# Performance work log

Measured on AMD Instinct MI355X. Metric: run time of the kernel, lower is better.

Reference implementation:

```python
import jax, jax.numpy as jnp
import numpy as np
from jax import lax

# PRPN (Parse-Read-Predict Network), eval mode (all dropout off, BatchNorm in eval
# with running stats mean=0/var=1, rmask=ones). Submodule math follows the upstream
# yikangshen/PRPN implementation vendored by jiant: ParsingNetwork (conv gate stack,
# hard hardtanh memory gates with cumprod over slots), ReadingNetwork (masked-softmax
# attention over nslots memory + LayerNorm LSTM cell, shift-append memory update),
# PredictNetwork (attention over prediction memory, res=0 -> Linear+BN+Tanh head).

T, B, V, D, H, S, L, NL = 192, 32, 50000, 384, 384, 15, 5, 2
RES = 0.1
G4 = 4 * H
BN_SC = np.float32(1.0 / np.sqrt(1.0 + 1e-5))   # eval BatchNorm with mean=0, var=1
INV_SQRT_H = np.float32(1.0 / np.sqrt(H))


def _layer_norm(x, g, b, eps=1e-6):
    # torch-style LayerNorm with unbiased std (x.std(-1))
    mu = jnp.mean(x, -1, keepdims=True)
    var = jnp.sum((x - mu) ** 2, -1, keepdims=True) / (x.shape[-1] - 1)
    return g * (x - mu) / (jnp.sqrt(var) + eps) + b


def _msoftmax(logits, gate, eps=1e-8):
    # blocks.softmax: exp-normalize then multiply by (soft) gate mask before sum
    e = jnp.exp(logits - jnp.max(logits, -1, keepdims=True)) * gate
    return e / (jnp.sum(e, -1, keepdims=True) + eps)


def _forward(input_ids, emb_w, pconv1_w, pconv1_b, pbn_g, pbn_b, pconv2_w, pconv2_b,
             r_wih, r_bih, r_whh, r_bhh, r_lnih_g, r_lnih_b, r_lnhh_g, r_lnhh_b,
             r_lnc_g, r_lnc_b, r_proj_w, r_proj_b,
             p_proj_w, p_proj_b, p_ffd_w, p_ffd_b, p_bn_g, p_bn_b):
    emb = emb_w[input_ids]                                        # (T,B,D)

    # ---- ParsingNetwork ----
    x = jnp.concatenate([jnp.zeros((L, B, D), emb.dtype), emb], 0)  # (T+L,B,D), zero history
    xc = jnp.transpose(x, (1, 2, 0))                              # (B,D,T+L)
    h1 = lax.conv_general_dilated(xc, pconv1_w, (1,), 'VALID',
                                  dimension_numbers=('NCH', 'OIH', 'NCH'))
    h1 = h1 + pconv1_b[None, :, None]
    h1 = jax.nn.relu(pbn_g[None, :, None] * h1 * BN_SC + pbn_b[None, :, None])  # (B,H,T)
    half = H // 2
    # Conv1d(nhid, 2, 1, groups=2): channel 0 from first half, channel 1 from second
    gate = jax.nn.sigmoid(jnp.einsum('bct,c->bt', h1[:, :half], pconv2_w[0]) + pconv2_b[0])
    gate_next = jax.nn.sigmoid(jnp.einsum('bct,c->bt', h1[:, half:], pconv2_w[1]) + pconv2_b[1])
    cum = jnp.concatenate([jnp.full((B, S), 1e9, gate.dtype), gate], 1)  # init cum_gate = +inf
    gate_hat = jnp.stack([cum[:, S - k:S - k + T] for k in range(S)], 2)  # (B,T,S)

    def mem_gate(g):  # hard gates: (hardtanh((g-ghat)/res*2+1)+1)/2, cumprod over slots
        u = (jnp.clip((g[:, :, None] - gate_hat) / RES * 2.0 + 1.0, -1.0, 1.0) + 1.0) * 0.5
        return jnp.cumprod(u, axis=2)

    mg = jnp.transpose(mem_gate(gate), (1, 0, 2))                 # (T,B,S)
    mgn = jnp.transpose(mem_gate(gate_next), (1, 0, 2))           # (T,B,S)

    # ---- per-timestep Read / Predict-attention loop ----
    def step(carry, xs):
        mem_h, mem_c, pmem = carry       # (NL,B,S,H),(NL,B,S,H),(B,S,H)
        e_t, mg_t, mgn_t = xs
        h = e_t
        nh, nc = [], []
        for j in range(NL):
            mh, mc = mem_h[j], mem_c[j]
            key_j = jnp.concatenate([h, mh[:, -1]], -1) @ r_proj_w[j].T + r_proj_b[j]
            att = _msoftmax(jnp.einsum('bsh,bh->bs', mh, key_j) * INV_SQRT_H, mg_t)
            sel_h = jnp.einsum('bs,bsh->bh', att, mh)
            sel_c = jnp.einsum('bs,bsh->bh', att, mc)
            gates = (_layer_norm(h @ r_wih[j].T + r_bih[j], r_lnih_g[j], r_lnih_b[j])
                     + _layer_norm(sel_h @ r_whh[j].T + r_bhh[j], r_lnhh_g[j], r_lnhh_b[j]))
            i_g, f_g, c_g, o_g = jnp.split(gates, 4, axis=-1)
            c_new = jax.nn.sigmoid(f_g) * sel_c + jax.nn.sigmoid(i_g) * jnp.tanh(c_g)
            h_new = jax.nn.sigmoid(o_g) * jnp.tanh(_layer_norm(c_new, r_lnc_g[j], r_lnc_b[j]))
            nh.append(jnp.concatenate([mh[:, 1:], h_new[:, None]], 1))
            nc.append(jnp.concatenate([mc[:, 1:], c_new[:, None]], 1))
            h = h_new
        pkey = jnp.concatenate([h, pmem[:, -1]], -1) @ p_proj_w.T + p_proj_b
        patt = _msoftmax(jnp.einsum('bsh,bh->bs', pmem, pkey) * INV_SQRT_H, mgn_t)
        sel = jnp.einsum('bs,bsh->bh', patt, pmem)
        pmem_new = jnp.concatenate([pmem[:, 1:], h[:, None]], 1)
        return (jnp.stack(nh), jnp.stack(nc), pmem_new), (h, sel)

    carry0 = (jnp.zeros((NL, B, S, H), emb.dtype),
              jnp.zeros((NL, B, S, H), emb.dtype),
              jnp.zeros((B, S, H), emb.dtype))
    _, (out_h, out_sel) = lax.scan(step, carry0, (emb, mg, mgn))

    # ---- PredictNetwork head (res=0): Linear(2H->D) + BN(eval) + Tanh ----
    flat = jnp.concatenate([out_h.reshape(T * B, H), out_sel.reshape(T * B, H)], -1)
    y = flat @ p_ffd_w.T + p_ffd_b
    y = jnp.tanh(p_bn_g * y * BN_SC + p_bn_b)
    return y.reshape(T, B, D)


def setup_inputs() -> dict:
    key = jax.random.key(0)
    ks = iter(jax.random.split(key, 16))

    def rn(shape, s=0.05):
        return jax.random.normal(next(ks), shape, dtype=jnp.float32) * s

    return {
        "input_ids": jax.random.randint(next(ks), (T, B), 0, V),
        "emb_w": rn((V, D), 0.01),
        "pconv1_w": rn((H, D, L + 1)),
        "pconv1_b": jnp.zeros((H,), jnp.float32),
        "pbn_g": jnp.ones((H,), jnp.float32),
        "pbn_b": jnp.zeros((H,), jnp.float32),
        "pconv2_w": rn((2, H // 2)),
        "pconv2_b": jnp.zeros((2,), jnp.float32),
        "r_wih": rn((NL, G4, D)),
        "r_bih": jnp.zeros((NL, G4), jnp.float32),
        "r_whh": rn((NL, G4, H)),
        "r_bhh": jnp.zeros((NL, G4), jnp.float32),
        "r_lnih_g": jnp.ones((NL, G4), jnp.float32),
        "r_lnih_b": jnp.zeros((NL, G4), jnp.float32),
        "r_lnhh_g": jnp.ones((NL, G4), jnp.float32),
        "r_lnhh_b": jnp.zeros((NL, G4), jnp.float32),
        "r_lnc_g": jnp.ones((NL, H), jnp.float32),
        "r_lnc_b": jnp.zeros((NL, H), jnp.float32),
        "r_proj_w": rn((NL, H, D + H)),
        "r_proj_b": jnp.zeros((NL, H), jnp.float32),
        "p_proj_w": rn((H, 2 * H)),
        "p_proj_b": jnp.zeros((H,), jnp.float32),
        "p_ffd_w": rn((D, 2 * H)),
        "p_ffd_b": jnp.zeros((D,), jnp.float32),
        "p_bn_g": jnp.ones((D,), jnp.float32),
        "p_bn_b": jnp.zeros((D,), jnp.float32),
    }


def reference(input_ids, emb_w, pconv1_w, pconv1_b, pbn_g, pbn_b, pconv2_w, pconv2_b,
              r_wih, r_bih, r_whh, r_bhh, r_lnih_g, r_lnih_b, r_lnhh_g, r_lnhh_b,
              r_lnc_g, r_lnc_b, r_proj_w, r_proj_b,
              p_proj_w, p_proj_b, p_ffd_w, p_ffd_b, p_bn_g, p_bn_b):
    out = _forward(input_ids, emb_w, pconv1_w, pconv1_b, pbn_g, pbn_b, pconv2_w, pconv2_b,
                   r_wih, r_bih, r_whh, r_bhh, r_lnih_g, r_lnih_b, r_lnhh_g, r_lnhh_b,
                   r_lnc_g, r_lnc_b, r_proj_w, r_proj_b,
                   p_proj_w, p_proj_b, p_ffd_w, p_ffd_b, p_bn_g, p_bn_b)
    mask = input_ids != 0
    return out, mask
```

## Files before the change

### kernel.cpp

```cpp
#include <hip/hip_runtime.h>


#define TT 192
#define TB 6144

constexpr size_t O_EMB    = 0;
constexpr size_t O_IH0LN  = 2359296;
constexpr size_t O_KEY0E  = 11796480;
constexpr size_t O_MG     = 14155776;
constexpr size_t O_MGN    = 14247936;
constexpr size_t O_H1     = 14340096;
constexpr size_t O_GATEA  = 16699392;
constexpr size_t O_GATEB  = 16705536;
constexpr size_t O_OUTHS  = 16711680;
constexpr size_t O_MEMH0  = 21430272;
constexpr size_t O_MEMC0  = 21614592;
constexpr size_t O_MEMH1  = 21798912;
constexpr size_t O_MEMC1  = 21983232;
constexpr size_t O_PMEM   = 22167552;
constexpr size_t O_P0     = 22351872;
constexpr size_t O_P1     = 23089152;
constexpr size_t O_HNEW0  = 23826432;
constexpr size_t O_HNEW1  = 23838720;
constexpr size_t O_IH1RAW = 23851008;
constexpr size_t O_KEY1H  = 23900160;
constexpr size_t O_KEY0MH = 23912448;
constexpr size_t O_KEY1MH = 23924736;
constexpr size_t O_PKEYH  = 23937024;
constexpr size_t O_PKEYMH = 23949312;
constexpr size_t O_BAR    = 23973888;
constexpr size_t O_WSEND  = 23974432;

__device__ __forceinline__ float sigmoidf(float x) { return 1.f / (1.f + expf(-x)); }

__device__ __forceinline__ float ldx(const float* p) {
  return __hip_atomic_load(p, __ATOMIC_RELAXED, __HIP_MEMORY_SCOPE_AGENT);
}
__device__ __forceinline__ void stx(float* p, float v) {
  __hip_atomic_store(p, v, __ATOMIC_RELAXED, __HIP_MEMORY_SCOPE_AGENT);
}
__device__ __forceinline__ unsigned ldu(const unsigned* p) {
  return __hip_atomic_load(p, __ATOMIC_RELAXED, __HIP_MEMORY_SCOPE_AGENT);
}

constexpr float BN_SC = 0.9999950000374997f;
constexpr float INV_SQRT_H = 0.05103103630798288f;

__device__ __forceinline__ float blockSum(float v, float* red) {
#pragma unroll
  for (int off = 32; off > 0; off >>= 1) v += __shfl_down(v, off, 64);
  __syncthreads();
  if ((threadIdx.x & 63) == 0) red[threadIdx.x >> 6] = v;
  __syncthreads();
  return red[0] + red[1] + red[2] + red[3];
}

__global__ __launch_bounds__(256) void k_zero(float* p, int n) {
  int i = blockIdx.x * 256 + threadIdx.x;
  int stride = gridDim.x * 256;
  for (; i < n; i += stride) p[i] = 0.f;
}

__global__ __launch_bounds__(256) void k_emb(const int* ids, const float* emb_w,
                                             float* emb, float* out) {
  size_t idx = (size_t)blockIdx.x * 256 + threadIdx.x;
  size_t stride = (size_t)gridDim.x * 256;
  for (size_t i = idx; i < (size_t)TB * 384; i += stride) {
    size_t tb = i / 384, d = i - tb * 384;
    int id = ids[tb];
    emb[i] = emb_w[(size_t)id * 384 + d];
    if (i < TB) out[(size_t)TB * 384 + i] = (ids[i] != 0) ? 1.f : 0.f;
  }
}

__global__ __launch_bounds__(256) void k_conv(const float* emb, const float* W1, const float* cbias,
                                              const float* bng, const float* bnb, float* h1) {
  __shared__ float As[32][68];
  __shared__ float Bs[32][68];
  int n0 = blockIdx.x * 64, m0 = blockIdx.y * 64;
  int tid = threadIdx.x;
  float acc[4][4] = {};
  int mi = tid >> 3, kq = tid & 7;
  int ni = tid >> 2, kb = tid & 3;
  for (int kk = 0; kk < 2304; kk += 32) {
    int kc = kk / 384, dbase = kk - kc * 384;
    __syncthreads();
#pragma unroll
    for (int p = 0; p < 2; ++p) {
      int m = m0 + mi + 32 * p;
      int b = m / 192, t = m - b * 192;
      int tt = t + kc - 5;
      float4 v = {0.f, 0.f, 0.f, 0.f};
      if (tt >= 0) v = *(const float4*)(emb + ((size_t)tt * 32 + b) * 384 + dbase + kq * 4);
      As[kq * 4 + 0][mi + 32 * p] = v.x; As[kq * 4 + 1][mi + 32 * p] = v.y;
      As[kq * 4 + 2][mi + 32 * p] = v.z; As[kq * 4 + 3][mi + 32 * p] = v.w;
    }
#pragma unroll
    for (int i = 0; i < 8; ++i) {
      int d = dbase + kb * 8 + i;
      Bs[kb * 8 + i][ni] = W1[(size_t)(n0 + ni) * 2304 + d * 6 + kc];
    }
    __syncthreads();
    int ty = tid >> 4, tx = tid & 15;
#pragma unroll
    for (int k = 0; k < 32; ++k) {
      float4 a = *(const float4*)(&As[k][ty * 4]);
      float4 bv = *(const float4*)(&Bs[k][tx * 4]);
// ... 93 lines not shown
  }
  int ty = tid >> 4, tx = tid & 15;
#pragma unroll
  for (int i = 0; i < 4; ++i) {
    int m = m0 + ty * 4 + i;
#pragma unroll
    for (int j = 0; j < 4; ++j) {
      int n = n0 + tx * 4 + j;
      float v = acc[i][j];
      if (bias) v += bias[n];
      if (mode == 0) Cf[(size_t)m * ldc + n] = v;
      else Cb[(size_t)m * ldc + n] = tanhf(bng[n] * v * BN_SC + bnb[n]);
    }
  }
}

__global__ __launch_bounds__(256) void k_ln_rows(float* X, const float* g, const float* bt) {
  __shared__ float red[8];
  float* x = X + (size_t)blockIdx.x * 1536;
  int tid = threadIdx.x;
  float ps = 0.f;
  for (int i = tid; i < 1536; i += 256) ps += x[i];
  float mu = blockSum(ps, red) * (1.f / 1536.f);
  ps = 0.f;
  for (int i = tid; i < 1536; i += 256) { float d = x[i] - mu; ps += d * d; }
  float inv = 1.f / (sqrtf(blockSum(ps, red) * (1.f / 1535.f)) + 1e-6f);
  for (int i = tid; i < 1536; i += 256) x[i] = g[i] * (x[i] - mu) * inv + bt[i];
}

struct ScanArgs {
  float* ws;
  const float *r_whh, *r_bhh, *r_lnhh_g, *r_lnhh_b, *r_lnih_g, *r_lnih_b;
  const float *r_lnc_g, *r_lnc_b, *r_wih, *r_bih, *r_proj_w, *r_proj_b;
  const float *p_proj_w, *p_proj_b;
};

struct GJob { const float* W; int ldw; int koff; const float* bias; float* dst; int rstride; int ncols; };

__device__ __forceinline__ void resolveJob(const GJob* J, int col, const float*& W, int& ldw, int& koff,
                                           const float*& bias, float*& dst, int& rstride, int& cc) {
  int c = col;
#pragma unroll
  for (int j = 0; j < 4; ++j) {
    if (c < J[j].ncols) {
      W = J[j].W; ldw = J[j].ldw; koff = J[j].koff; bias = J[j].bias;
      dst = J[j].dst; rstride = J[j].rstride; cc = c; return;
    }
    c -= J[j].ncols;
  }
  W = J[0].W; ldw = J[0].ldw; koff = J[0].koff; bias = J[0].bias;
  dst = J[0].dst; rstride = J[0].rstride; cc = 0;
}

__device__ void grid_barrier(unsigned* bar, int wg, unsigned k) {
  __syncthreads();
  if (threadIdx.x == 0) {
    const int g = wg >> 4;
    unsigned arr = __hip_atomic_fetch_add(bar + g * 16, 1u, __ATOMIC_RELAXED, __HIP_MEMORY_SCOPE_AGENT);
    if (arr == k * 16u + 15u) {
      unsigned ra = __hip_atomic_fetch_add(bar + 256, 1u, __ATOMIC_RELAXED, __HIP_MEMORY_SCOPE_AGENT);
      if (ra == k * 16u + 15u) {
        __hip_atomic_store(bar + 272, k + 1u, __ATOMIC_RELAXED, __HIP_MEMORY_SCOPE_AGENT);
      } else {
        while (ldu(bar + 272) < k + 1u) __builtin_amdgcn_s_sleep(2);
      }
      __hip_atomic_store(bar + 288 + g * 16, k + 1u, __ATOMIC_RELAXED, __HIP_MEMORY_SCOPE_AGENT);
    } else {
      while (ldu(bar + 288 + g * 16) < k + 1u) __builtin_amdgcn_s_sleep(8);
    }
  }
  __syncthreads();
}

#define NG_GEMV 224
__device__ void gemm_phase(const float* src, const GJob* J, int NC, int gwg,
                           float* xs , float* red ) {
  const int tid = threadIdx.x;
  for (int j = tid; j < 12288; j += 256) {
    int bb = j >> 8;
    bb = j / 384;
    int kk = j - bb * 384;
    xs[bb * 385 + kk] = ldx(src + j);
  }
  __syncthreads();
  const int b = tid & 31, cg = tid >> 5;
  const int c0 = (gwg * NC) / NG_GEMV, c1 = ((gwg + 1) * NC) / NG_GEMV;
  const int colsPer = c1 - c0;
  const int k0 = cg * 48;
  float xr[48];
  const float* xp = xs + b * 385 + k0;
#pragma unroll
  for (int q = 0; q < 48; ++q) xr[q] = xp[q];
  for (int ci = 0; ci < colsPer; ++ci) {
    const float* W; int ldw, koff; const float* bias; float* dst; int rstride; int cc;
    resolveJob(J, c0 + ci, W, ldw, koff, bias, dst, rstride, cc);
    const float* wr = W + (size_t)cc * ldw + koff + k0;
    float a = 0.f;
#pragma unroll
    for (int q = 0; q < 12; ++q) {
      float4 w = *(const float4*)(wr + q * 4);
      a += w.x * xr[q * 4 + 0] + w.y * xr[q * 4 + 1]
         + w.z * xr[q * 4 + 2] + w.w * xr[q * 4 + 3];
    }
    red[(cg * colsPer + ci) * 33 + b] = a;
  }
  __syncthreads();
  const int pairs = colsPer * 32;
  for (int pi = tid; pi < pairs; pi += 256) {
    int bb = pi / colsPer, ci = pi - bb * colsPer;
    float s = 0.f;
#pragma unroll
    for (int g = 0; g < 8; ++g) s += red[(g * colsPer + ci) * 33 + bb];
    const float* W; int ldw, koff; const float* bias; float* dst; int rstride; int cc;
    resolveJob(J, c0 + ci, W, ldw, koff, bias, dst, rstride, cc);
    if (bias) s += bias[cc];
    stx(dst + (size_t)bb * rstride + cc, s);
  }
  __syncthreads();
}

__device__ void per_b_layer(int layer, int t, int b, const ScanArgs& A, float* sm) {
  float* ws = A.ws;
  const int tid = threadIdx.x;
  const size_t tb = (size_t)t * 32 + b;
  float* memh = ws + (layer ? O_MEMH1 : O_MEMH0) + (size_t)b * 15 * 384;
  float* memc = ws + (layer ? O_MEMC1 : O_MEMC0) + (size_t)b * 15 * 384;
  float* P = ws + (layer ? O_P1 : O_P0) + (size_t)b * 15 * 1536;
  float* keyl = sm; float* logit = sm + 384; float* att = sm + 400; float* red = sm + 416;
  float* ghh = sm + 448; float* gih = sm + 1984; float* selc = sm + 3520;
  float* cnew = sm + 3904; float* ogat = sm + 4288;

  for (int h = tid; h < 384; h += 256) {
    float k1, k2;
    if (layer == 0) { k1 = ws[O_KEY0E + tb * 384 + h]; k2 = ldx(ws + O_KEY0MH + (size_t)b * 384 + h); }
    else { k1 = ldx(ws + O_KEY1H + (size_t)b * 384 + h); k2 = ldx(ws + O_KEY1MH + (size_t)b * 384 + h); }
    keyl[h] = k1 + k2;
  }
  __syncthreads();
  {
    int s = tid >> 4, l = tid & 15;
    if (s < 15) {
      const float* mh = memh + ((t + s) % 15) * 384;
      float p = 0.f;
      for (int k = l; k < 384; k += 16) p += mh[k] * keyl[k];
      p += __shfl_down(p, 8, 64); p += __shfl_down(p, 4, 64);
      p += __shfl_down(p, 2, 64); p += __shfl_down(p, 1, 64);
      if (l == 0) logit[s] = p * INV_SQRT_H;
    }
  }
  __syncthreads();
  if (tid == 0) {
    const float* mgp = ws + O_MG + tb * 15;
    float m = logit[0];
    for (int i = 1; i < 15; ++i) m = fmaxf(m, logit[i]);
    float sum = 0.f;
    for (int i = 0; i < 15; ++i) { float e = expf(logit[i] - m) * mgp[i]; att[i] = e; sum += e; }
    float inv = 1.f / (sum + 1e-8f);
    for (int i = 0; i < 15; ++i) att[i] *= inv;
  }
  __syncthreads();
  float av[15]; int pidx[15];
#pragma unroll
  for (int i = 0; i < 15; ++i) { av[i] = att[i]; pidx[i] = (t + i) % 15; }
  const float* bhh = A.r_bhh + layer * 1536;
  for (int n = tid; n < 1536; n += 256) {
    float acc = bhh[n];
#pragma unroll
    for (int i = 0; i < 15; ++i) acc += av[i] * ldx(P + (size_t)pidx[i] * 1536 + n);
    ghh[n] = acc;
  }
  for (int h = tid; h < 384; h += 256) {
    float acc = 0.f;
#pragma unroll
    for (int i = 0; i < 15; ++i) acc += av[i] * memc[pidx[i] * 384 + h];
    selc[h] = acc;
  }
  if (layer) {
    for (int n = tid; n < 1536; n += 256) gih[n] = ldx(ws + O_IH1RAW + (size_t)b * 1536 + n);
  }
  __syncthreads();
  float ps = 0.f;
  for (int n = tid; n < 1536; n += 256) ps += ghh[n];
  float mu_hh = blockSum(ps, red) * (1.f / 1536.f);
  ps = 0.f;
  for (int n = tid; n < 1536; n += 256) { float d = ghh[n] - mu_hh; ps += d * d; }
  float inv_hh = 1.f / (sqrtf(blockSum(ps, red) * (1.f / 1535.f)) + 1e-6f);
  float mu_ih = 0.f, inv_ih = 0.f;
  if (layer) {
    ps = 0.f;
    for (int n = tid; n < 1536; n += 256) ps += gih[n];
    mu_ih = blockSum(ps, red) * (1.f / 1536.f);
    ps = 0.f;
    for (int n = tid; n < 1536; n += 256) { float d = gih[n] - mu_ih; ps += d * d; }
    inv_ih = 1.f / (sqrtf(blockSum(ps, red) * (1.f / 1535.f)) + 1e-6f);
  }
  const float *hg = A.r_lnhh_g + layer * 1536, *hb = A.r_lnhh_b + layer * 1536;
  const float *ig = A.r_lnih_g + 1536, *ib = A.r_lnih_b + 1536;
  for (int h = tid; h < 384; h += 256) {
    float gi, gf, gc, go;
    if (layer == 0) {
      const float* ihr = ws + O_IH0LN + tb * 1536;
      gi = ihr[h]; gf = ihr[384 + h]; gc = ihr[768 + h]; go = ihr[1152 + h];
    } else {
      gi = ig[h] * (gih[h] - mu_ih) * inv_ih + ib[h];
      gf = ig[384 + h] * (gih[384 + h] - mu_ih) * inv_ih + ib[384 + h];
      gc = ig[768 + h] * (gih[768 + h] - mu_ih) * inv_ih + ib[768 + h];
      go = ig[1152 + h] * (gih[1152 + h] - mu_ih) * inv_ih + ib[1152 + h];
    }
    gi += hg[h] * (ghh[h] - mu_hh) * inv_hh + hb[h];
    gf += hg[384 + h] * (ghh[384 + h] - mu_hh) * inv_hh + hb[384 + h];
    gc += hg[768 + h] * (ghh[768 + h] - mu_hh) * inv_hh + hb[768 + h];
    go += hg[1152 + h] * (ghh[1152 + h] - mu_hh) * inv_hh + hb[1152 + h];
    float c = sigmoidf(gf) * selc[h] + sigmoidf(gi) * tanhf(gc);
    cnew[h] = c; ogat[h] = go;
  }
  __syncthreads();
  ps = 0.f;
  for (int h = tid; h < 384; h += 256) ps += cnew[h];
  float mu_c = blockSum(ps, red) * (1.f / 384.f);
  ps = 0.f;
  for (int h = tid; h < 384; h += 256) { float d = cnew[h] - mu_c; ps += d * d; }
  float inv_c = 1.f / (sqrtf(blockSum(ps, red) * (1.f / 383.f)) + 1e-6f);
  const float *lcg = A.r_lnc_g + layer * 384, *lcb = A.r_lnc_b + layer * 384;
  const int slot = t % 15;
  for (int h = tid; h < 384; h += 256) {
    float hn = sigmoidf(ogat[h]) * tanhf(lcg[h] * (cnew[h] - mu_c) * inv_c + lcb[h]);
    memh[slot * 384 + h] = hn;
    memc[slot * 384 + h] = cnew[h];
    if (layer == 0) stx(ws + O_HNEW0 + (size_t)b * 384 + h, hn);
    else { stx(ws + O_HNEW1 + (size_t)b * 384 + h, hn); ws[O_OUTHS + tb * 768 + h] = hn; }
  }
}

__device__ void per_b_predict(int tau, int b, const ScanArgs& A, float* sm) {
  float* ws = A.ws;
  const int tid = threadIdx.x;
  const size_t tb = (size_t)tau * 32 + b;
  float* pmem = ws + O_PMEM + (size_t)b * 15 * 384;
  float* keyl = sm; float* logit = sm + 384; float* att = sm + 400;
  for (int h = tid; h < 384; h += 256)
    keyl[h] = ldx(ws + O_PKEYH + (size_t)b * 384 + h)
            + ldx(ws + O_PKEYMH + (size_t)(tau & 1) * 12288 + (size_t)b * 384 + h);
  __syncthreads();
  {
    int s = tid >> 4, l = tid & 15;
    if (s < 15) {
      const float* mh = pmem + ((tau + s) % 15) * 384;
      float p = 0.f;
      for (int k = l; k < 384; k += 16) p += mh[k] * keyl[k];
      p += __shfl_down(p, 8, 64); p += __shfl_down(p, 4, 64);
      p += __shfl_down(p, 2, 64); p += __shfl_down(p, 1, 64);
      if (l == 0) logit[s] = p * INV_SQRT_H;
    }
  }
  __syncthreads();
  if (tid == 0) {
    const float* mgp = ws + O_MGN + tb * 15;
    float m = logit[0];
    for (int i = 1; i < 15; ++i) m = fmaxf(m, logit[i]);
    float sum = 0.f;
    for (int i = 0; i < 15; ++i) { float e = expf(logit[i] - m) * mgp[i]; att[i] = e; sum += e; }
    float inv = 1.f / (sum + 1e-8f);
    for (int i = 0; i < 15; ++i) att[i] *= inv;
  }
  __syncthreads();
  float av[15]; int pidx[15];
#pragma unroll
  for (int i = 0; i < 15; ++i) { av[i] = att[i]; pidx[i] = (tau + i) % 15; }
  for (int h = tid; h < 384; h += 256) {
    float acc = 0.f;
#pragma unroll
    for (int i = 0; i < 15; ++i) acc += av[i] * pmem[pidx[i] * 384 + h];
    ws[O_OUTHS + tb * 768 + 384 + h] = acc;
  }
  __syncthreads();
  for (int h = tid; h < 384; h += 256)
    pmem[(tau % 15) * 384 + h] = ldx(ws + O_HNEW1 + (size_t)b * 384 + h);
}

__global__ __launch_bounds__(256) void k_scan(ScanArgs A) {
  __shared__ float sm[16032];
  float* ws = A.ws;
  unsigned* bar = (unsigned*)(ws + O_BAR);
  const int wg = blockIdx.x;
  float* xs = sm;
  float* red = sm + 12320;
  unsigned bk = 0;
  for (int t = 0; t <= TT; ++t) {
    if (wg < 32) {
      if (t < TT) per_b_layer(0, t, wg, A, sm);
    } else {
      GJob J[4] = {
        { A.r_whh + 589824, 384, 0, nullptr, ws + O_P1 + (size_t)((t + 14) % 15) * 1536, 23040, 1536 },
        { A.r_proj_w + 294912, 768, 384, nullptr, ws + O_KEY1MH, 384, 384 },
        { A.p_proj_w, 768, 0, A.p_proj_b, ws + O_PKEYH, 384, 384 },
        { A.p_proj_w, 768, 384, nullptr, ws + O_PKEYMH + (size_t)(t & 1) * 12288, 384, 384 },
      };
      gemm_phase(ws + O_HNEW1, J, 2688, wg - 32, xs, red);
    }
    grid_barrier(bar, wg, bk); ++bk;
    if (wg < 32) {
      if (t >= 1) per_b_predict(t - 1, wg, A, sm);
    } else if (t < TT) {
      GJob J[4] = {
        { A.r_wih + 589824, 384, 0, A.r_bih + 1536, ws + O_IH1RAW, 1536, 1536 },
        { A.r_proj_w + 294912, 768, 0, A.r_proj_b + 384, ws + O_KEY1H, 384, 384 },
        { nullptr, 0, 0, nullptr, nullptr, 0, 0 },
        { nullptr, 0, 0, nullptr, nullptr, 0, 0 },
      };
      gemm_phase(ws + O_HNEW0, J, 1920, wg - 32, xs, red);
    }
    if (t == TT) break;
    grid_barrier(bar, wg, bk); ++bk;
    if (wg < 32) {
      per_b_layer(1, t, wg, A, sm);
    } else {
      GJob J[4] = {
        { A.r_whh, 384, 0, nullptr, ws + O_P0 + (size_t)(t % 15) * 1536, 23040, 1536 },
        { A.r_proj_w, 768, 384, nullptr, ws + O_KEY0MH, 384, 384 },
        { nullptr, 0, 0, nullptr, nullptr, 0, 0 },
        { nullptr, 0, 0, nullptr, nullptr, 0, 0 },
      };
      gemm_phase(ws + O_HNEW0, J, 1920, wg - 32, xs, red);
    }
    grid_barrier(bar, wg, bk); ++bk;
  }
}

extern "C" void kernel_launch(void* const* d_in, const int* in_sizes, int n_in,
                              void* d_out, int out_size, void* d_ws, size_t ws_size,
                              hipStream_t stream) {
  const int* ids = (const int*)d_in[0];
  const float* emb_w = (const float*)d_in[1];
  const float* pconv1_w = (const float*)d_in[2];
  const float* pconv1_b = (const float*)d_in[3];
  const float* pbn_g = (const float*)d_in[4];
  const float* pbn_b = (const float*)d_in[5];
  const float* pconv2_w = (const float*)d_in[6];
  const float* pconv2_b = (const float*)d_in[7];
  const float* r_wih = (const float*)d_in[8];
  const float* r_bih = (const float*)d_in[9];
  const float* r_whh = (const float*)d_in[10];
  const float* r_bhh = (const float*)d_in[11];
  const float* r_lnih_g = (const float*)d_in[12];
  const float* r_lnih_b = (const float*)d_in[13];
  const float* r_lnhh_g = (const float*)d_in[14];
  const float* r_lnhh_b = (const float*)d_in[15];
  const float* r_lnc_g = (const float*)d_in[16];
  const float* r_lnc_b = (const float*)d_in[17];
  const float* r_proj_w = (const float*)d_in[18];
  const float* r_proj_b = (const float*)d_in[19];
  const float* p_proj_w = (const float*)d_in[20];
  const float* p_proj_b = (const float*)d_in[21];
  const float* p_ffd_w = (const float*)d_in[22];
  const float* p_ffd_b = (const float*)d_in[23];
  const float* p_bn_g = (const float*)d_in[24];
  const float* p_bn_b = (const float*)d_in[25];
  float* ws = (float*)d_ws;
  float* out = (float*)d_out;

  k_zero<<<1024, 256, 0, stream>>>(ws + O_MEMH0, (int)(O_WSEND - O_MEMH0));
  k_emb<<<4096, 256, 0, stream>>>(ids, emb_w, ws + O_EMB, out);
  k_conv<<<dim3(6, 96), 256, 0, stream>>>(ws + O_EMB, pconv1_w, pconv1_b, pbn_g, pbn_b, ws + O_H1);
  k_gate<<<6144, 256, 0, stream>>>(ws + O_H1, pconv2_w, pconv2_b, ws + O_GATEA, ws + O_GATEB);
  k_mg<<<24, 256, 0, stream>>>(ws + O_GATEA, ws + O_GATEB, ws + O_MG, ws + O_MGN);
  k_gemm<<<dim3(24, 96), 256, 0, stream>>>(ws + O_EMB, 384, r_wih, 384, r_bih,
                                           ws + O_IH0LN, 1536, 384, 0, nullptr, nullptr, nullptr);
  k_gemm<<<dim3(6, 96), 256, 0, stream>>>(ws + O_EMB, 384, r_proj_w, 768, r_proj_b,
                                          ws + O_KEY0E, 384, 384, 0, nullptr, nullptr, nullptr);
  k_ln_rows<<<6144, 256, 0, stream>>>(ws + O_IH0LN, r_lnih_g, r_lnih_b);
  ScanArgs SA{ws, r_whh, r_bhh, r_lnhh_g, r_lnhh_b, r_lnih_g, r_lnih_b,
              r_lnc_g, r_lnc_b, r_wih, r_bih, r_proj_w, r_proj_b, p_proj_w, p_proj_b};
  k_scan<<<256, 256, 0, stream>>>(SA);
  k_gemm<<<dim3(6, 96), 256, 0, stream>>>(ws + O_OUTHS, 768, p_ffd_w, 768, p_ffd_b,
                                          nullptr, 384, 768, 1, p_bn_g, p_bn_b, out);
}
```

Before: 14.24 ms.

## Pipeline LSTM layers and predict across workgroup sets with split producer/consumer barriers

New measurement: 16.21 ms. +13.9%, slower.

```diff
diff --git a/kernel.cpp b/kernel.cpp
--- a/kernel.cpp
+++ b/kernel.cpp
@@ -3,6 +3,7 @@
 
 #define TT 192
 #define TB 6144
+#define NGV 160
 
 constexpr size_t O_EMB    = 0;
 constexpr size_t O_IH0LN  = 2359296;
@@ -21,7 +22,8 @@
 constexpr size_t O_P0     = 22351872;
 constexpr size_t O_P1     = 23089152;
 constexpr size_t O_HNEW0  = 23826432;
-constexpr size_t O_HNEW1  = 23838720;
+constexpr size_t O_HNEW1A = 23838720;
+constexpr size_t O_HNEW1B = 14340096;
 constexpr size_t O_IH1RAW = 23851008;
 constexpr size_t O_KEY1H  = 23900160;
 constexpr size_t O_KEY0MH = 23912448;
@@ -30,6 +32,13 @@
 constexpr size_t O_PKEYMH = 23949312;
 constexpr size_t O_BAR    = 23973888;
 constexpr size_t O_WSEND  = 23974432;
+
+#define BO_GRP_E  0
+#define BO_ROOT_E 96
+#define BO_GEN_E  112
+#define BO_GRP_O  128
+#define BO_ROOT_O 288
+#define BO_GEN_O  304
 
 __device__ __forceinline__ float sigmoidf(float x) { return 1.f / (1.f + expf(-x)); }
 
@@ -252,49 +261,28 @@
   dst = J[0].dst; rstride = J[0].rstride; cc = 0;
 }
 
-__device__ void grid_barrier(unsigned* bar, int wg, unsigned k) {
-  __syncthreads();
-  if (threadIdx.x == 0) {
-    const int g = wg >> 4;
-    unsigned arr = __hip_atomic_fetch_add(bar + g * 16, 1u, __ATOMIC_RELAXED, __HIP_MEMORY_SCOPE_AGENT);
-    if (arr == k * 16u + 15u) {
-      unsigned ra = __hip_atomic_fetch_add(bar + 256, 1u, __ATOMIC_RELAXED, __HIP_MEMORY_SCOPE_AGENT);
-      if (ra == k * 16u + 15u) {
-        __hip_atomic_store(bar + 272, k + 1u, __ATOMIC_RELAXED, __HIP_MEMORY_SCOPE_AGENT);
-      } else {
-        while (ldu(bar + 272) < k + 1u) __builtin_amdgcn_s_sleep(2);
-      }
-      __hip_atomic_store(bar + 288 + g * 16, k + 1u, __ATOMIC_RELAXED, __HIP_MEMORY_SCOPE_AGENT);
-    } else {
-      while (ldu(bar + 288 + g * 16) < k + 1u) __builtin_amdgcn_s_sleep(8);
-    }
-  }
-  __syncthreads();
-}
-
-#define NG_GEMV 224
-__device__ void gemm_phase(const float* src, const GJob* J, int NC, int gwg,
-                           float* xs , float* red ) {
+__device__ __forceinline__ void arrive2(unsigned* bar, int grpOff, int rootOff, int genOff,
+                                        int g, int ngroups, unsigned s) {
+  unsigned a = __hip_atomic_fetch_add(bar + grpOff + g * 16, 1u, __ATOMIC_RELAXED, __HIP_MEMORY_SCOPE_AGENT);
+  if (a == s * 16u + 15u) {
+    unsigned r = __hip_atomic_fetch_add(bar + rootOff, 1u, __ATOMIC_RELAXED, __HIP_MEMORY_SCOPE_AGENT);
+    if (r == s * (unsigned)ngroups + (unsigned)(ngroups - 1))
+      __hip_atomic_store(bar + genOff, s + 1u, __ATOMIC_RELAXED, __HIP_MEMORY_SCOPE_AGENT);
+  }
+}
+__device__ __forceinline__ void waitgen(const unsigned* bar, int genOff, unsigned tgt) {
+  while (ldu(bar + genOff) < tgt) __builtin_amdgcn_s_sleep(2);
+}
+
+__device__ void gemv_half(const GJob* J, int NC, int gwg, const float* xr, float* red) {
   const int tid = threadIdx.x;
-  for (int j = tid; j < 12288; j += 256) {
-    int bb = j >> 8;
-    bb = j / 384;
-    int kk = j - bb * 384;
-    xs[bb * 385 + kk] = ldx(src + j);
-  }
-  __syncthreads();
   const int b = tid & 31, cg = tid >> 5;
-  const int c0 = (gwg * NC) / NG_GEMV, c1 = ((gwg + 1) * NC) / NG_GEMV;
-  const int colsPer = c1 - c0;
-  const int k0 = cg * 48;
-  float xr[48];
-  const float* xp = xs + b * 385 + k0;
-#pragma unroll
-  for (int q = 0; q < 48; ++q) xr[q] = xp[q];
-  for (int ci = 0; ci < colsPer; ++ci) {
+  const int c0 = (gwg * NC) / NGV, c1 = ((gwg + 1) * NC) / NGV;
+  const int nch = c1 - c0;
+  for (int ci = 0; ci < nch; ++ci) {
     const float* W; int ldw, koff; const float* bias; float* dst; int rstride; int cc;
     resolveJob(J, c0 + ci, W, ldw, koff, bias, dst, rstride, cc);
-    const float* wr = W + (size_t)cc * ldw + koff + k0;
+    const float* wr = W + (size_t)cc * ldw + koff + cg * 48;
     float a = 0.f;
 #pragma unroll
     for (int q = 0; q < 12; ++q) {
@@ -302,19 +290,20 @@
       a += w.x * xr[q * 4 + 0] + w.y * xr[q * 4 + 1]
          + w.z * xr[q * 4 + 2] + w.w * xr[q * 4 + 3];
     }
-    red[(cg * colsPer + ci) * 33 + b] = a;
-  }
-  __syncthreads();
-  const int pairs = colsPer * 32;
+    a += __shfl_down(a, 32, 64);
+    if ((cg & 1) == 0) red[((cg >> 1) * nch + ci) * 33 + b] = a;
+  }
+  __syncthreads();
+  const int pairs = nch * 32;
   for (int pi = tid; pi < pairs; pi += 256) {
-    int bb = pi / colsPer, ci = pi - bb * colsPer;
-    float s = 0.f;
-#pragma unroll
-    for (int g = 0; g < 8; ++g) s += red[(g * colsPer + ci) * 33 + bb];
+    int bb = pi / nch, ci = pi - bb * nch;
+    float ssum = 0.f;
+#pragma unroll
+    for (int g2 = 0; g2 < 4; ++g2) ssum += red[(g2 * nch + ci) * 33 + bb];
     const float* W; int ldw, koff; const float* bias; float* dst; int rstride; int cc;
     resolveJob(J, c0 + ci, W, ldw, koff, bias, dst, rstride, cc);
-    if (bias) s += bias[cc];
-    stx(dst + (size_t)bb * rstride + cc, s);
+    if (bias) ssum += bias[cc];
+    stx(dst + (size_t)bb * rstride + cc, ssum);
   }
   __syncthreads();
 }
@@ -336,6 +325,11 @@
     else { k1 = ldx(ws + O_KEY1H + (size_t)b * 384 + h); k2 = ldx(ws + O_KEY1MH + (size_t)b * 384 + h); }
     keyl[h] = k1 + k2;
   }
+  if (layer) {
+    for (int n = tid; n < 1536; n += 256) gih[n] = ldx(ws + O_IH1RAW + (size_t)b * 1536 + n);
+  } else {
+    for (int n = tid; n < 1536; n += 256) gih[n] = ws[O_IH0LN + tb * 1536 + n];
+  }
   __syncthreads();
   {
     int s = tid >> 4, l = tid & 15;
@@ -374,9 +368,6 @@
 #pragma unroll
     for (int i = 0; i < 15; ++i) acc += av[i] * memc[pidx[i] * 384 + h];
     selc[h] = acc;
-  }
-  if (layer) {
-    for (int n = tid; n < 1536; n += 256) gih[n] = ldx(ws + O_IH1RAW + (size_t)b * 1536 + n);
   }
   __syncthreads();
   float ps = 0.f;
@@ -399,8 +390,7 @@
   for (int h = tid; h < 384; h += 256) {
     float gi, gf, gc, go;
     if (layer == 0) {
-      const float* ihr = ws + O_IH0LN + tb * 1536;
-      gi = ihr[h]; gf = ihr[384 + h]; gc = ihr[768 + h]; go = ihr[1152 + h];
+      gi = gih[h]; gf = gih[384 + h]; gc = gih[768 + h]; go = gih[1152 + h];
     } else {
       gi = ig[h] * (gih[h] - mu_ih) * inv_ih + ib[h];
       gf = ig[384 + h] * (gih[384 + h] - mu_ih) * inv_ih + ib[384 + h];
@@ -427,8 +417,12 @@
     float hn = sigmoidf(ogat[h]) * tanhf(lcg[h] * (cnew[h] - mu_c) * inv_c + lcb[h]);
     memh[slot * 384 + h] = hn;
     memc[slot * 384 + h] = cnew[h];
-    if (layer == 0) stx(ws + O_HNEW0 + (size_t)b * 384 + h, hn);
-    else { stx(ws + O_HNEW1 + (size_t)b * 384 + h, hn); ws[O_OUTHS + tb * 768 + h] = hn; }
+    if (layer == 0) {
+      stx(ws + O_HNEW0 + (size_t)b * 384 + h, hn);
+    } else {
+      stx(ws + ((t & 1) ? O_HNEW1B : O_HNEW1A) + (size_t)b * 384 + h, hn);
+      ws[O_OUTHS + tb * 768 + h] = hn;
+    }
   }
 }
 
@@ -475,55 +469,101 @@
   }
   __syncthreads();
   for (int h = tid; h < 384; h += 256)
-    pmem[(tau % 15) * 384 + h] = ldx(ws + O_HNEW1 + (size_t)b * 384 + h);
+    pmem[(tau % 15) * 384 + h] = ldx(ws + ((tau & 1) ? O_HNEW1B : O_HNEW1A) + (size_t)b * 384 + h);
 }
 
 __global__ __launch_bounds__(256) void k_scan(ScanArgs A) {
-  __shared__ float sm[16032];
+  __shared__ float sm[15488];
   float* ws = A.ws;
   unsigned* bar = (unsigned*)(ws + O_BAR);
   const int wg = blockIdx.x;
-  float* xs = sm;
-  float* red = sm + 12320;
-  unsigned bk = 0;
-  for (int t = 0; t <= TT; ++t) {
-    if (wg < 32) {
-      if (t < TT) per_b_layer(0, t, wg, A, sm);
-    } else {
-      GJob J[4] = {
-        { A.r_whh + 589824, 384, 0, nullptr, ws + O_P1 + (size_t)((t + 14) % 15) * 1536, 23040, 1536 },
-        { A.r_proj_w + 294912, 768, 384, nullptr, ws + O_KEY1MH, 384, 384 },
-        { A.p_proj_w, 768, 0, A.p_proj_b, ws + O_PKEYH, 384, 384 },
-        { A.p_proj_w, 768, 384, nullptr, ws + O_PKEYMH + (size_t)(t & 1) * 12288, 384, 384 },
-      };
-      gemm_phase(ws + O_HNEW1, J, 2688, wg - 32, xs, red);
-    }
-    grid_barrier(bar, wg, bk); ++bk;
-    if (wg < 32) {
-      if (t >= 1) per_b_predict(t - 1, wg, A, sm);
-    } else if (t < TT) {
-      GJob J[4] = {
-        { A.r_wih + 589824, 384, 0, A.r_bih + 1536, ws + O_IH1RAW, 1536, 1536 },
-        { A.r_proj_w + 294912, 768, 0, A.r_proj_b + 384, ws + O_KEY1H, 384, 384 },
-        { nullptr, 0, 0, nullptr, nullptr, 0, 0 },
-        { nullptr, 0, 0, nullptr, nullptr, 0, 0 },
-      };
-      gemm_phase(ws + O_HNEW0, J, 1920, wg - 32, xs, red);
-    }
-    if (t == TT) break;
-    grid_barrier(bar, wg, bk); ++bk;
-    if (wg < 32) {
-      per_b_layer(1, t, wg, A, sm);
-    } else {
-      GJob J[4] = {
-        { A.r_whh, 384, 0, nullptr, ws + O_P0 + (size_t)(t % 15) * 1536, 23040, 1536 },
-        { A.r_proj_w, 768, 384, nullptr, ws + O_KEY0MH, 384, 384 },
-        { nullptr, 0, 0, nullptr, nullptr, 0, 0 },
-        { nullptr, 0, 0, nullptr, nullptr, 0, 0 },
-      };
-      gemm_phase(ws + O_HNEW0, J, 1920, wg - 32, xs, red);
-    }
-    grid_barrier(bar, wg, bk); ++bk;
+  const int tid = threadIdx.x;
+
+  if (wg < 96) {
+    const int g = wg >> 4;
+    for (int s = 0; s < 194; ++s) {
+      if (wg < 32) {
+        if (s < 192) per_b_layer(0, s, wg, A, sm);
+      } else if (wg < 64) {
+        if (s >= 1 && s <= 192) per_b_layer(1, s - 1, wg - 32, A, sm);
+      } else {
+        if (s >= 2) per_b_predict(s - 2, wg - 64, A, sm);
+      }
+      __syncthreads();
+      if (tid == 0) {
+        arrive2(bar, BO_GRP_E, BO_ROOT_E, BO_GEN_E, g, 6, (unsigned)s);
+        if (s < 193) waitgen(bar, BO_GEN_O, (unsigned)s + 1);
+      }
+      __syncthreads();
+    }
+  } else {
+    const int gwg = wg - 96;
+    const int g = gwg >> 4;
+    float* xs = sm;
+    float* red = sm + 12320;
+    const int b = tid & 31, cg = tid >> 5;
+    const float* xp = xs + b * 385 + cg * 48;
+    for (int s = 0; s < 193; ++s) {
+      if (tid == 0) waitgen(bar, BO_GEN_E, (unsigned)s + 1);
+      __syncthreads();
+      const bool doG0 = (s < 192), doG1 = (s >= 1);
+      const float* src1 = ws + (((s - 1) & 1) ? O_HNEW1B : O_HNEW1A);
+      float xr[48];
+      if (doG0) {
+        for (int j = tid; j < 12288; j += 256) {
+          int bb = j / 384, kk = j - bb * 384;
+          xs[bb * 385 + kk] = ldx(ws + O_HNEW0 + j);
+        }
+        __syncthreads();
+#pragma unroll
+        for (int q = 0; q < 48; ++q) xr[q] = xp[q];
+        float x1v[48];
+        if (doG1) {
+#pragma unroll
+          for (int q = 0; q < 48; ++q) x1v[q] = ldx(src1 + tid + q * 256);
+        }
+        __syncthreads();
+        {
+          GJob J0[4] = {
+            { A.r_wih + 589824, 384, 0, A.r_bih + 1536, ws + O_IH1RAW, 1536, 1536 },
+            { A.r_proj_w + 294912, 768, 0, A.r_proj_b + 384, ws + O_KEY1H, 384, 384 },
+            { A.r_whh, 384, 0, nullptr, ws + O_P0 + (size_t)(s % 15) * 1536, 23040, 1536 },
+            { A.r_proj_w, 768, 384, nullptr, ws + O_KEY0MH, 384, 384 },
+          };
+          gemv_half(J0, 3840, gwg, xr, red);
+        }
+        if (doG1) {
+#pragma unroll
+          for (int q = 0; q < 48; ++q) {
+            int j = tid + q * 256;
+            int bb = j / 384, kk = j - bb * 384;
+            xs[bb * 385 + kk] = x1v[q];
+          }
+          __syncthreads();
+#pragma unroll
+          for (int q = 0; q < 48; ++q) xr[q] = xp[q];
+        }
+      } else {
+        for (int j = tid; j < 12288; j += 256) {
+          int bb = j / 384, kk = j - bb * 384;
+          xs[bb * 385 + kk] = ldx(src1 + j);
+        }
+        __syncthreads();
+#pragma unroll
+        for (int q = 0; q < 48; ++q) xr[q] = xp[q];
+      }
+      if (doG1) {
+        GJob J1[4] = {
+          { A.r_whh + 589824, 384, 0, nullptr, ws + O_P1 + (size_t)((s + 14) % 15) * 1536, 23040, 1536 },
+          { A.r_proj_w + 294912, 768, 384, nullptr, ws + O_KEY1MH, 384, 384 },
+          { A.p_proj_w, 768, 0, A.p_proj_b, ws + O_PKEYH, 384, 384 },
+          { A.p_proj_w, 768, 384, nullptr, ws + O_PKEYMH + (size_t)(s & 1) * 12288, 384, 384 },
+        };
+        gemv_half(J1, 2688, gwg, xr, red);
+      }
+      __syncthreads();
+      if (tid == 0) arrive2(bar, BO_GRP_O, BO_ROOT_O, BO_GEN_O, g, 10, (unsigned)s);
+    }
   }
 }
 
```

## Split scan workgroups by role, stage gate GEMV outputs, and vectorize per-batch steps

Applied to the files above, without the earlier changes.

Result: no change. 14.31 ms (+0.5%).

```diff
diff --git a/kernel.cpp b/kernel.cpp
--- a/kernel.cpp
+++ b/kernel.cpp
@@ -3,6 +3,7 @@
 
 #define TT 192
 #define TB 6144
+#define NGV 192
 
 constexpr size_t O_EMB    = 0;
 constexpr size_t O_IH0LN  = 2359296;
@@ -10,6 +11,8 @@
 constexpr size_t O_MG     = 14155776;
 constexpr size_t O_MGN    = 14247936;
 constexpr size_t O_H1     = 14340096;
+constexpr size_t O_P0S    = 14340096;
+constexpr size_t O_P1S    = 14389248;
 constexpr size_t O_GATEA  = 16699392;
 constexpr size_t O_GATEB  = 16705536;
 constexpr size_t O_OUTHS  = 16711680;
@@ -39,6 +42,15 @@
 __device__ __forceinline__ void stx(float* p, float v) {
   __hip_atomic_store(p, v, __ATOMIC_RELAXED, __HIP_MEMORY_SCOPE_AGENT);
 }
+__device__ __forceinline__ float2 ldx2(const float* p) {
+  unsigned long long v = __hip_atomic_load((const unsigned long long*)p,
+                                           __ATOMIC_RELAXED, __HIP_MEMORY_SCOPE_AGENT);
+  return __builtin_bit_cast(float2, v);
+}
+__device__ __forceinline__ void stx2(float* p, float2 v) {
+  __hip_atomic_store((unsigned long long*)p, __builtin_bit_cast(unsigned long long, v),
+                     __ATOMIC_RELAXED, __HIP_MEMORY_SCOPE_AGENT);
+}
 __device__ __forceinline__ unsigned ldu(const unsigned* p) {
   return __hip_atomic_load(p, __ATOMIC_RELAXED, __HIP_MEMORY_SCOPE_AGENT);
 }
@@ -53,6 +65,19 @@
   if ((threadIdx.x & 63) == 0) red[threadIdx.x >> 6] = v;
   __syncthreads();
   return red[0] + red[1] + red[2] + red[3];
+}
+
+__device__ __forceinline__ float2 blockSum2(float a, float b, float* red) {
+#pragma unroll
+  for (int off = 32; off > 0; off >>= 1) {
+    a += __shfl_down(a, off, 64);
+    b += __shfl_down(b, off, 64);
+  }
+  __syncthreads();
+  if ((threadIdx.x & 63) == 0) { int w = threadIdx.x >> 6; red[2 * w] = a; red[2 * w + 1] = b; }
+  __syncthreads();
+  return make_float2(red[0] + red[2] + red[4] + red[6],
+                     red[1] + red[3] + red[5] + red[7]);
 }
 
 __global__ __launch_bounds__(256) void k_zero(float* p, int n) {
@@ -266,25 +291,24 @@
       }
       __hip_atomic_store(bar + 288 + g * 16, k + 1u, __ATOMIC_RELAXED, __HIP_MEMORY_SCOPE_AGENT);
     } else {
-      while (ldu(bar + 288 + g * 16) < k + 1u) __builtin_amdgcn_s_sleep(8);
-    }
-  }
-  __syncthreads();
-}
-
-#define NG_GEMV 224
-__device__ void gemm_phase(const float* src, const GJob* J, int NC, int gwg,
+      while (ldu(bar + 288 + g * 16) < k + 1u) __builtin_amdgcn_s_sleep(4);
+    }
+  }
+  __syncthreads();
+}
+
+__device__ void gemv_phase(const float* src, const GJob* J, int NC, int gwg,
                            float* xs , float* red ) {
   const int tid = threadIdx.x;
-  for (int j = tid; j < 12288; j += 256) {
-    int bb = j >> 8;
-    bb = j / 384;
-    int kk = j - bb * 384;
-    xs[bb * 385 + kk] = ldx(src + j);
+  for (int j2 = tid; j2 < 6144; j2 += 256) {
+    int j = j2 * 2;
+    int bb = j / 384, kk = j - bb * 384;
+    float2 v = ldx2(src + j);
+    xs[bb * 385 + kk] = v.x; xs[bb * 385 + kk + 1] = v.y;
   }
   __syncthreads();
   const int b = tid & 31, cg = tid >> 5;
-  const int c0 = (gwg * NC) / NG_GEMV, c1 = ((gwg + 1) * NC) / NG_GEMV;
+  const int c0 = (gwg * NC) / NGV, c1 = ((gwg + 1) * NC) / NGV;
   const int colsPer = c1 - c0;
   const int k0 = cg * 48;
   float xr[48];
@@ -319,23 +343,56 @@
   __syncthreads();
 }
 
+__device__ void preload_l0(int t, int b, const ScanArgs& A, float* sm) {
+  float* ws = A.ws;
+  const int tid = threadIdx.x;
+  const size_t tb = (size_t)t * 32 + b;
+  float* keyl = sm; float* gih = sm + 1984;
+  for (int n = tid; n < 1536; n += 256) gih[n] = ws[O_IH0LN + tb * 1536 + n];
+  if (tid < 192) {
+    float2 v = *(const float2*)(ws + O_KEY0E + tb * 384 + 2 * tid);
+    keyl[2 * tid] = v.x; keyl[2 * tid + 1] = v.y;
+  }
+}
+
 __device__ void per_b_layer(int layer, int t, int b, const ScanArgs& A, float* sm) {
   float* ws = A.ws;
   const int tid = threadIdx.x;
   const size_t tb = (size_t)t * 32 + b;
   float* memh = ws + (layer ? O_MEMH1 : O_MEMH0) + (size_t)b * 15 * 384;
   float* memc = ws + (layer ? O_MEMC1 : O_MEMC0) + (size_t)b * 15 * 384;
-  float* P = ws + (layer ? O_P1 : O_P0) + (size_t)b * 15 * 1536;
+  float* mir  = ws + (layer ? O_P1 : O_P0) + (size_t)b * 23040;
+  const float* stg = ws + (layer ? O_P1S : O_P0S) + (size_t)b * 1536;
   float* keyl = sm; float* logit = sm + 384; float* att = sm + 400; float* red = sm + 416;
   float* ghh = sm + 448; float* gih = sm + 1984; float* selc = sm + 3520;
   float* cnew = sm + 3904; float* ogat = sm + 4288;
 
-  for (int h = tid; h < 384; h += 256) {
-    float k1, k2;
-    if (layer == 0) { k1 = ws[O_KEY0E + tb * 384 + h]; k2 = ldx(ws + O_KEY0MH + (size_t)b * 384 + h); }
-    else { k1 = ldx(ws + O_KEY1H + (size_t)b * 384 + h); k2 = ldx(ws + O_KEY1MH + (size_t)b * 384 + h); }
-    keyl[h] = k1 + k2;
-  }
+  const int pslot = (t + 14) % 15;
+#pragma unroll
+  for (int i = 0; i < 3; ++i) {
+    int idx = tid + i * 256;
+    float2 v = ldx2(stg + 2 * idx);
+    *(float2*)(mir + (size_t)pslot * 1536 + 2 * idx) = v;
+  }
+  if (layer == 0) {
+    if (tid < 192) {
+      float2 c = ldx2(ws + O_KEY0MH + (size_t)b * 384 + 2 * tid);
+      keyl[2 * tid] += c.x; keyl[2 * tid + 1] += c.y;
+    }
+  } else {
+#pragma unroll
+    for (int i = 0; i < 3; ++i) {
+      int idx = tid + i * 256;
+      float2 v = ldx2(ws + O_IH1RAW + (size_t)b * 1536 + 2 * idx);
+      gih[2 * idx] = v.x; gih[2 * idx + 1] = v.y;
+    }
+    if (tid < 192) {
+      float2 a = ldx2(ws + O_KEY1H + (size_t)b * 384 + 2 * tid);
+      float2 c = ldx2(ws + O_KEY1MH + (size_t)b * 384 + 2 * tid);
+      keyl[2 * tid] = a.x + c.x; keyl[2 * tid + 1] = a.y + c.y;
+    }
+  }
+  float mgv = (tid < 15) ? ws[O_MG + tb * 15 + tid] : 0.f;
   __syncthreads();
   {
     int s = tid >> 4, l = tid & 15;
@@ -349,14 +406,17 @@
     }
   }
   __syncthreads();
-  if (tid == 0) {
-    const float* mgp = ws + O_MG + tb * 15;
-    float m = logit[0];
-    for (int i = 1; i < 15; ++i) m = fmaxf(m, logit[i]);
-    float sum = 0.f;
-    for (int i = 0; i < 15; ++i) { float e = expf(logit[i] - m) * mgp[i]; att[i] = e; sum += e; }
-    float inv = 1.f / (sum + 1e-8f);
-    for (int i = 0; i < 15; ++i) att[i] *= inv;
+  if (tid < 64) {
+    float lg = (tid < 15) ? logit[tid] : -3.0e38f;
+    lg = fmaxf(lg, __shfl_xor(lg, 8, 64));
+    lg = fmaxf(lg, __shfl_xor(lg, 4, 64));
+    lg = fmaxf(lg, __shfl_xor(lg, 2, 64));
+    lg = fmaxf(lg, __shfl_xor(lg, 1, 64));
+    float e = (tid < 15) ? expf(logit[tid] - lg) * mgv : 0.f;
+    float ssum = e;
+    ssum += __shfl_xor(ssum, 1, 64); ssum += __shfl_xor(ssum, 2, 64);
+    ssum += __shfl_xor(ssum, 4, 64); ssum += __shfl_xor(ssum, 8, 64);
+    if (tid < 15) att[tid] = e / (ssum + 1e-8f);
   }
   __syncthreads();
   float av[15]; int pidx[15];
@@ -366,7 +426,7 @@
   for (int n = tid; n < 1536; n += 256) {
     float acc = bhh[n];
 #pragma unroll
-    for (int i = 0; i < 15; ++i) acc += av[i] * ldx(P + (size_t)pidx[i] * 1536 + n);
+    for (int i = 0; i < 15; ++i) acc += av[i] * mir[(size_t)pidx[i] * 1536 + n];
     ghh[n] = acc;
   }
   for (int h = tid; h < 384; h += 256) {
@@ -375,32 +435,26 @@
     for (int i = 0; i < 15; ++i) acc += av[i] * memc[pidx[i] * 384 + h];
     selc[h] = acc;
   }
-  if (layer) {
-    for (int n = tid; n < 1536; n += 256) gih[n] = ldx(ws + O_IH1RAW + (size_t)b * 1536 + n);
-  }
-  __syncthreads();
-  float ps = 0.f;
-  for (int n = tid; n < 1536; n += 256) ps += ghh[n];
-  float mu_hh = blockSum(ps, red) * (1.f / 1536.f);
-  ps = 0.f;
-  for (int n = tid; n < 1536; n += 256) { float d = ghh[n] - mu_hh; ps += d * d; }
-  float inv_hh = 1.f / (sqrtf(blockSum(ps, red) * (1.f / 1535.f)) + 1e-6f);
+  __syncthreads();
+  float s1 = 0.f, s2 = 0.f;
+  for (int n = tid; n < 1536; n += 256) { float v = ghh[n]; s1 += v; s2 += v * v; }
+  float2 rhh = blockSum2(s1, s2, red);
+  float mu_hh = rhh.x * (1.f / 1536.f);
+  float inv_hh = 1.f / (sqrtf(fmaxf(rhh.y - rhh.x * mu_hh, 0.f) * (1.f / 1535.f)) + 1e-6f);
   float mu_ih = 0.f, inv_ih = 0.f;
   if (layer) {
-    ps = 0.f;
-    for (int n = tid; n < 1536; n += 256) ps += gih[n];
-    mu_ih = blockSum(ps, red) * (1.f / 1536.f);
-    ps = 0.f;
-    for (int n = tid; n < 1536; n += 256) { float d = gih[n] - mu_ih; ps += d * d; }
-    inv_ih = 1.f / (sqrtf(blockSum(ps, red) * (1.f / 1535.f)) + 1e-6f);
+    s1 = 0.f; s2 = 0.f;
+    for (int n = tid; n < 1536; n += 256) { float v = gih[n]; s1 += v; s2 += v * v; }
+    float2 rih = blockSum2(s1, s2, red);
+    mu_ih = rih.x * (1.f / 1536.f);
+    inv_ih = 1.f / (sqrtf(fmaxf(rih.y - rih.x * mu_ih, 0.f) * (1.f / 1535.f)) + 1e-6f);
   }
   const float *hg = A.r_lnhh_g + layer * 1536, *hb = A.r_lnhh_b + layer * 1536;
   const float *ig = A.r_lnih_g + 1536, *ib = A.r_lnih_b + 1536;
   for (int h = tid; h < 384; h += 256) {
     float gi, gf, gc, go;
     if (layer == 0) {
-      const float* ihr = ws + O_IH0LN + tb * 1536;
-      gi = ihr[h]; gf = ihr[384 + h]; gc = ihr[768 + h]; go = ihr[1152 + h];
+      gi = gih[h]; gf = gih[384 + h]; gc = gih[768 + h]; go = gih[1152 + h];
     } else {
       gi = ig[h] * (gih[h] - mu_ih) * inv_ih + ib[h];
       gf = ig[384 + h] * (gih[384 + h] - mu_ih) * inv_ih + ib[384 + h];
@@ -415,20 +469,22 @@
     cnew[h] = c; ogat[h] = go;
   }
   __syncthreads();
-  ps = 0.f;
-  for (int h = tid; h < 384; h += 256) ps += cnew[h];
-  float mu_c = blockSum(ps, red) * (1.f / 384.f);
-  ps = 0.f;
-  for (int h = tid; h < 384; h += 256) { float d = cnew[h] - mu_c; ps += d * d; }
-  float inv_c = 1.f / (sqrtf(blockSum(ps, red) * (1.f / 383.f)) + 1e-6f);
+  s1 = 0.f; s2 = 0.f;
+  for (int h = tid; h < 384; h += 256) { float v = cnew[h]; s1 += v; s2 += v * v; }
+  float2 rc = blockSum2(s1, s2, red);
+  float mu_c = rc.x * (1.f / 384.f);
+  float inv_c = 1.f / (sqrtf(fmaxf(rc.y - rc.x * mu_c, 0.f) * (1.f / 383.f)) + 1e-6f);
   const float *lcg = A.r_lnc_g + layer * 384, *lcb = A.r_lnc_b + layer * 384;
   const int slot = t % 15;
-  for (int h = tid; h < 384; h += 256) {
-    float hn = sigmoidf(ogat[h]) * tanhf(lcg[h] * (cnew[h] - mu_c) * inv_c + lcb[h]);
-    memh[slot * 384 + h] = hn;
-    memc[slot * 384 + h] = cnew[h];
-    if (layer == 0) stx(ws + O_HNEW0 + (size_t)b * 384 + h, hn);
-    else { stx(ws + O_HNEW1 + (size_t)b * 384 + h, hn); ws[O_OUTHS + tb * 768 + h] = hn; }
+  if (tid < 192) {
+    int h0 = 2 * tid, h1 = h0 + 1;
+    float c0 = cnew[h0], c1 = cnew[h1];
+    float hn0 = sigmoidf(ogat[h0]) * tanhf(lcg[h0] * (c0 - mu_c) * inv_c + lcb[h0]);
+    float hn1 = sigmoidf(ogat[h1]) * tanhf(lcg[h1] * (c1 - mu_c) * inv_c + lcb[h1]);
+    *(float2*)(memh + slot * 384 + h0) = make_float2(hn0, hn1);
+    *(float2*)(memc + slot * 384 + h0) = make_float2(c0, c1);
+    stx2(ws + (layer ? O_HNEW1 : O_HNEW0) + (size_t)b * 384 + h0, make_float2(hn0, hn1));
+    if (layer) *(float2*)(ws + O_OUTHS + tb * 768 + h0) = make_float2(hn0, hn1);
   }
 }
 
@@ -437,10 +493,14 @@
   const int tid = threadIdx.x;
   const size_t tb = (size_t)tau * 32 + b;
   float* pmem = ws + O_PMEM + (size_t)b * 15 * 384;
+  const float* memh1 = ws + O_MEMH1 + (size_t)b * 15 * 384;
   float* keyl = sm; float* logit = sm + 384; float* att = sm + 400;
-  for (int h = tid; h < 384; h += 256)
-    keyl[h] = ldx(ws + O_PKEYH + (size_t)b * 384 + h)
-            + ldx(ws + O_PKEYMH + (size_t)(tau & 1) * 12288 + (size_t)b * 384 + h);
+  if (tid < 192) {
+    float2 a = ldx2(ws + O_PKEYH + (size_t)b * 384 + 2 * tid);
+    float2 c = ldx2(ws + O_PKEYMH + (size_t)(tau & 1) * 12288 + (size_t)b * 384 + 2 * tid);
+    keyl[2 * tid] = a.x + c.x; keyl[2 * tid + 1] = a.y + c.y;
+  }
+  float mgv = (tid < 15) ? ws[O_MGN + tb * 15 + tid] : 0.f;
   __syncthreads();
   {
     int s = tid >> 4, l = tid & 15;
@@ -454,14 +514,17 @@
     }
   }
   __syncthreads();
-  if (tid == 0) {
-    const float* mgp = ws + O_MGN + tb * 15;
-    float m = logit[0];
-    for (int i = 1; i < 15; ++i) m = fmaxf(m, logit[i]);
-    float sum = 0.f;
-    for (int i = 0; i < 15; ++i) { float e = expf(logit[i] - m) * mgp[i]; att[i] = e; sum += e; }
-    float inv = 1.f / (sum + 1e-8f);
-    for (int i = 0; i < 15; ++i) att[i] *= inv;
+  if (tid < 64) {
+    float lg = (tid < 15) ? logit[tid] : -3.0e38f;
+    lg = fmaxf(lg, __shfl_xor(lg, 8, 64));
+    lg = fmaxf(lg, __shfl_xor(lg, 4, 64));
+    lg = fmaxf(lg, __shfl_xor(lg, 2, 64));
+    lg = fmaxf(lg, __shfl_xor(lg, 1, 64));
+    float e = (tid < 15) ? expf(logit[tid] - lg) * mgv : 0.f;
+    float ssum = e;
+    ssum += __shfl_xor(ssum, 1, 64); ssum += __shfl_xor(ssum, 2, 64);
+    ssum += __shfl_xor(ssum, 4, 64); ssum += __shfl_xor(ssum, 8, 64);
+    if (tid < 15) att[tid] = e / (ssum + 1e-8f);
   }
   __syncthreads();
   float av[15]; int pidx[15];
@@ -474,8 +537,11 @@
     ws[O_OUTHS + tb * 768 + 384 + h] = acc;
   }
   __syncthreads();
-  for (int h = tid; h < 384; h += 256)
-    pmem[(tau % 15) * 384 + h] = ldx(ws + O_HNEW1 + (size_t)b * 384 + h);
+  if (tid < 192) {
+    const int slot = tau % 15;
+    *(float2*)(pmem + slot * 384 + 2 * tid) =
+        *(const float2*)(memh1 + slot * 384 + 2 * tid);
+  }
 }
 
 __global__ __launch_bounds__(256) void k_scan(ScanArgs A) {
@@ -486,42 +552,45 @@
   float* xs = sm;
   float* red = sm + 12320;
   unsigned bk = 0;
+  if (wg < 32) preload_l0(0, wg, A, sm);
   for (int t = 0; t <= TT; ++t) {
     if (wg < 32) {
       if (t < TT) per_b_layer(0, t, wg, A, sm);
-    } else {
+    } else if (wg >= 64) {
       GJob J[4] = {
-        { A.r_whh + 589824, 384, 0, nullptr, ws + O_P1 + (size_t)((t + 14) % 15) * 1536, 23040, 1536 },
+        { A.r_whh + 589824, 384, 0, nullptr, ws + O_P1S, 1536, 1536 },
         { A.r_proj_w + 294912, 768, 384, nullptr, ws + O_KEY1MH, 384, 384 },
         { A.p_proj_w, 768, 0, A.p_proj_b, ws + O_PKEYH, 384, 384 },
         { A.p_proj_w, 768, 384, nullptr, ws + O_PKEYMH + (size_t)(t & 1) * 12288, 384, 384 },
       };
-      gemm_phase(ws + O_HNEW1, J, 2688, wg - 32, xs, red);
+      gemv_phase(ws + O_HNEW1, J, 2688, wg - 64, xs, red);
     }
     grid_barrier(bar, wg, bk); ++bk;
-    if (wg < 32) {
-      if (t >= 1) per_b_predict(t - 1, wg, A, sm);
-    } else if (t < TT) {
+    if (wg >= 32 && wg < 64) {
+      if (t >= 1) per_b_predict(t - 1, wg - 32, A, sm);
+    } else if (wg >= 64 && t < TT) {
       GJob J[4] = {
         { A.r_wih + 589824, 384, 0, A.r_bih + 1536, ws + O_IH1RAW, 1536, 1536 },
         { A.r_proj_w + 294912, 768, 0, A.r_proj_b + 384, ws + O_KEY1H, 384, 384 },
         { nullptr, 0, 0, nullptr, nullptr, 0, 0 },
         { nullptr, 0, 0, nullptr, nullptr, 0, 0 },
       };
-      gemm_phase(ws + O_HNEW0, J, 1920, wg - 32, xs, red);
+      gemv_phase(ws + O_HNEW0, J, 1920, wg - 64, xs, red);
     }
     if (t == TT) break;
     grid_barrier(bar, wg, bk); ++bk;
-    if (wg < 32) {
-      per_b_layer(1, t, wg, A, sm);
+    if (wg >= 32 && wg < 64) {
+      per_b_layer(1, t, wg - 32, A, sm);
+    } else if (wg < 32) {
+      if (t + 1 < TT) preload_l0(t + 1, wg, A, sm);
     } else {
       GJob J[4] = {
-        { A.r_whh, 384, 0, nullptr, ws + O_P0 + (size_t)(t % 15) * 1536, 23040, 1536 },
+        { A.r_whh, 384, 0, nullptr, ws + O_P0S, 1536, 1536 },
         { A.r_proj_w, 768, 384, nullptr, ws + O_KEY0MH, 384, 384 },
         { nullptr, 0, 0, nullptr, nullptr, 0, 0 },
         { nullptr, 0, 0, nullptr, nullptr, 0, 0 },
       };
-      gemm_phase(ws + O_HNEW0, J, 1920, wg - 32, xs, red);
+      gemv_phase(ws + O_HNEW0, J, 1920, wg - 64, xs, red);
     }
     grid_barrier(bar, wg, bk); ++bk;
   }
@@ -564,6 +633,7 @@
   k_conv<<<dim3(6, 96), 256, 0, stream>>>(ws + O_EMB, pconv1_w, pconv1_b, pbn_g, pbn_b, ws + O_H1);
   k_gate<<<6144, 256, 0, stream>>>(ws + O_H1, pconv2_w, pconv2_b, ws + O_GATEA, ws + O_GATEB);
   k_mg<<<24, 256, 0, stream>>>(ws + O_GATEA, ws + O_GATEB, ws + O_MG, ws + O_MGN);
+  k_zero<<<96, 256, 0, stream>>>(ws + O_P0S, 98304);
   k_gemm<<<dim3(24, 96), 256, 0, stream>>>(ws + O_EMB, 384, r_wih, 384, r_bih,
                                            ws + O_IH0LN, 1536, 384, 0, nullptr, nullptr, nullptr);
   k_gemm<<<dim3(6, 96), 256, 0, stream>>>(ws + O_EMB, 384, r_proj_w, 768, r_proj_b,
```
